# Kernel tuning notes

Measured on AMD Instinct MI355X. Metric: run time of the kernel, lower is better.

Reference implementation:

```python
import jax, jax.numpy as jnp
import numpy as np

N = 65536   # batch of (state, goal) pairs
S = 256     # s_dim
G = 128     # goal_dim
L = 128     # latent_dim (prior units[-1] == rvq dim)
A = 32      # action_dim
H = 512     # prior/posterior hidden
DH = 1024   # decoder hidden
Q = 8       # num residual quantizers
K = 1024    # codebook size


def setup_inputs() -> dict:
    key = jax.random.key(0)
    ks = jax.random.split(key, 16)

    def w(k, i, o):
        return jax.random.normal(k, (i, o), jnp.float32) * (1.0 / np.sqrt(i))

    return {
        "s": jax.random.normal(ks[0], (N, S), jnp.float32),
        "goal": jax.random.normal(ks[1], (N, G), jnp.float32),
        # PriorNet: S -> H -> H -> L (relu between, linear last)
        "pW0": w(ks[2], S, H), "pb0": jnp.zeros((H,), jnp.float32),
        "pW1": w(ks[3], H, H), "pb1": jnp.zeros((H,), jnp.float32),
        "pW2": w(ks[4], H, L), "pb2": jnp.zeros((L,), jnp.float32),
        # PosteriorNet: (S+G) -> H -> H -> L
        "qW0": w(ks[5], S + G, H), "qb0": jnp.zeros((H,), jnp.float32),
        "qW1": w(ks[6], H, H), "qb1": jnp.zeros((H,), jnp.float32),
        "qW2": w(ks[7], H, L), "qb2": jnp.zeros((L,), jnp.float32),
        # ActionDecoder: (S+L) -> DH -> DH (relu after each) -> mu_head A
        "dW0": w(ks[8], S + L, DH), "db0": jnp.zeros((DH,), jnp.float32),
        "dW1": w(ks[9], DH, DH), "db1": jnp.zeros((DH,), jnp.float32),
        "dW2": w(ks[10], DH, A), "db2": jnp.zeros((A,), jnp.float32),
        # per-quantizer codebooks [Q, K, L]
        "codebooks": jax.random.normal(ks[11], (Q, K, L), jnp.float32) * 0.02,
    }


def _rvq(y, codebooks):
    """Residual VQ with straight-through estimator.
    y: [N, L]; codebooks: [Q, K, L]. Returns (y_hat [N,L], loss_vq scalar)."""
    def step(carry, cb):
        residual, out = carry
        # argmin_k ||residual - cb[k]||^2 (drop the ||residual||^2 term)
        d = jnp.sum(cb * cb, axis=-1)[None, :] - 2.0 * (residual @ cb.T)  # [N, K]
        idx = jnp.argmin(d, axis=-1)                                       # [N]
        quant = cb[idx]                                                    # [N, L] gather
        quant_st = residual + jax.lax.stop_gradient(quant - residual)      # straight-through
        commit = jnp.mean((jax.lax.stop_gradient(quant) - residual) ** 2)  # commitment loss
        new_res = residual - jax.lax.stop_gradient(quant)
        return (new_res, out + quant_st), commit

    (_, y_hat), commits = jax.lax.scan(step, (y, jnp.zeros_like(y)), codebooks)
    return y_hat, jnp.sum(commits)


def reference(s, goal,
              pW0, pb0, pW1, pb1, pW2, pb2,
              qW0, qb0, qW1, qb1, qW2, qb2,
              dW0, db0, dW1, db1, dW2, db2,
              codebooks):
    relu = jax.nn.relu
    # prior: zp = f_theta(s)
    h = relu(s @ pW0 + pb0)
    h = relu(h @ pW1 + pb1)
    zp = h @ pW2 + pb2                                  # [N, L]
    # posterior: z = f_phi(s, goal)
    x = jnp.concatenate([s, goal], axis=-1)
    h = relu(x @ qW0 + qb0)
    h = relu(h @ qW1 + qb1)
    z = h @ qW2 + qb2                                   # [N, L]
    zp_sg = jax.lax.stop_gradient(zp)
    y = z - zp_sg
    y_hat, loss_vq = _rvq(y, codebooks)
    z_hat = y_hat + zp_sg
    # decoder: a_hat = pi_low(s, z_hat)
    xd = jnp.concatenate([s, z_hat], axis=-1)
    h = relu(xd @ dW0 + db0)
    h = relu(h @ dW1 + db1)
    a_hat = h @ dW2 + db2                               # [N, A]
    return a_hat
```

## Files before the change

kernel.cpp:

```cpp
#include <hip/hip_runtime.h>

#define NROWS 65536
typedef unsigned short u16;
typedef __attribute__((ext_vector_type(8))) short bf16x8;
typedef __attribute__((ext_vector_type(4))) float f32x4;

__device__ __forceinline__ u16 tobf(float v) {
    unsigned b = __float_as_uint(v);
    b += 0x7fffu + ((b >> 16) & 1u);
    return (u16)(b >> 16);
}
__device__ __forceinline__ float frombf(u16 h) {
    return __uint_as_float(((unsigned)h) << 16);
}
__device__ __forceinline__ void split2(float v, u16& h, u16& l) {
    h = tobf(v);
    l = tobf(v - frombf(h));
}

__global__ __launch_bounds__(256)
void wsplit(const float* __restrict__ W, u16* __restrict__ Th, u16* __restrict__ Tl,
            int K, int N)
{
    __shared__ float Tt[32][65];
    const int t = threadIdx.x;
    const int nb = blockIdx.x * 32, kb = blockIdx.y * 64;
    #pragma unroll
    for (int j = 0; j < 2; ++j) {
        int fi = j * 256 + t;
        int kk = fi >> 3;
        int n4 = (fi & 7) * 4;
        float4 v = *(const float4*)&W[(size_t)(kb + kk) * N + nb + n4];
        Tt[n4 + 0][kk] = v.x; Tt[n4 + 1][kk] = v.y;
        Tt[n4 + 2][kk] = v.z; Tt[n4 + 3][kk] = v.w;
    }
    __syncthreads();
    #pragma unroll
    for (int j = 0; j < 2; ++j) {
        int oi = j * 256 + t;
        int n  = oi >> 4;
        int k4 = (oi & 15) * 4;
        ushort4 h, l;
        split2(Tt[n][k4 + 0], h.x, l.x); split2(Tt[n][k4 + 1], h.y, l.y);
        split2(Tt[n][k4 + 2], h.z, l.z); split2(Tt[n][k4 + 3], h.w, l.w);
        size_t oa = (size_t)(nb + n) * K + kb + k4;
        *(ushort4*)(Th + oa) = h;
        *(ushort4*)(Tl + oa) = l;
    }
}

template<int FM, int FN, int NWX, int NWY, int RELU>
__global__ __launch_bounds__(256)
void gemm3(const float* __restrict__ A1, int w1,
           const float* __restrict__ A2, int w2,
           const u16* __restrict__ Wth, const u16* __restrict__ Wtl,
           const float* __restrict__ bias,
           float* __restrict__ C, int Kin, int Nout)
{
    constexpr int BM = NWY * FM * 16;
    constexpr int BN = NWX * FN * 16;
    constexpr int LDT = 40;
    static_assert(NWX * NWY == 4, "4 waves");
    __shared__ u16 Ah[BM * LDT], Al[BM * LDT], Bh[BN * LDT], Bl[BN * LDT];

    const int t = threadIdx.x, lane = t & 63, w = t >> 6;
    const int wx = w % NWX, wy = w / NWX;
    const int lg = lane >> 4, lm = lane & 15;
    const int rbase = blockIdx.y * BM, cbase = blockIdx.x * BN;

    f32x4 acc[FM][FN];
    #pragma unroll
    for (int i = 0; i < FM; ++i)
        #pragma unroll
        for (int j = 0; j < FN; ++j) acc[i][j] = (f32x4){0.f, 0.f, 0.f, 0.f};

    for (int kb = 0; kb < Kin; kb += 32) {
        #pragma unroll
        for (int j = 0; j < BM / 32; ++j) {
            int fi  = j * 256 + t;
            int row = fi >> 3;
            int k   = (fi & 7) * 4;
            int gc  = kb + k;
            const float* src = (gc < w1) ? (A1 + (size_t)(rbase + row) * w1 + gc)
                                         : (A2 + (size_t)(rbase + row) * w2 + (gc - w1));
            float4 v = *(const float4*)src;
            ushort4 h, l;
            split2(v.x, h.x, l.x); split2(v.y, h.y, l.y);
            split2(v.z, h.z, l.z); split2(v.w, h.w, l.w);
            *(ushort4*)&Ah[row * LDT + k] = h;
            *(ushort4*)&Al[row * LDT + k] = l;
        }
        #pragma unroll
        for (int j = 0; j < BN / 32; ++j) {
            int fi   = j * 256 + t;
            int nrow = fi >> 3;
            int k    = (fi & 7) * 4;
            size_t ga = (size_t)(cbase + nrow) * Kin + kb + k;
            *(ushort4*)&Bh[nrow * LDT + k] = *(const ushort4*)(Wth + ga);
            *(ushort4*)&Bl[nrow * LDT + k] = *(const ushort4*)(Wtl + ga);
        }
        __syncthreads();

        bf16x8 a_h[FM], a_l[FM], b_h[FN], b_l[FN];
        #pragma unroll
        for (int fm = 0; fm < FM; ++fm) {
            int off = (wy * FM * 16 + fm * 16 + lm) * LDT + lg * 8;
            a_h[fm] = *(const bf16x8*)&Ah[off];
            a_l[fm] = *(const bf16x8*)&Al[off];
        }
        #pragma unroll
        for (int fn = 0; fn < FN; ++fn) {
            int off = (wx * FN * 16 + fn * 16 + lm) * LDT + lg * 8;
            b_h[fn] = *(const bf16x8*)&Bh[off];
            b_l[fn] = *(const bf16x8*)&Bl[off];
        }
        #pragma unroll
        for (int fm = 0; fm < FM; ++fm)
            #pragma unroll
            for (int fn = 0; fn < FN; ++fn) {
                acc[fm][fn] = __builtin_amdgcn_mfma_f32_16x16x32_bf16(a_h[fm], b_h[fn], acc[fm][fn], 0, 0, 0);
                acc[fm][fn] = __builtin_amdgcn_mfma_f32_16x16x32_bf16(a_h[fm], b_l[fn], acc[fm][fn], 0, 0, 0);
                acc[fm][fn] = __builtin_amdgcn_mfma_f32_16x16x32_bf16(a_l[fm], b_h[fn], acc[fm][fn], 0, 0, 0);
            }
        __syncthreads();
    }

    float bn_[FN];
    #pragma unroll
    for (int fn = 0; fn < FN; ++fn)
        bn_[fn] = bias[cbase + wx * FN * 16 + fn * 16 + lm];
    #pragma unroll
    for (int fm = 0; fm < FM; ++fm)
        #pragma unroll
        for (int fn = 0; fn < FN; ++fn)
            #pragma unroll
            for (int r = 0; r < 4; ++r) {
                int m = rbase + wy * FM * 16 + fm * 16 + lg * 4 + r;
                int n = cbase + wx * FN * 16 + fn * 16 + lm;
                float v = acc[fm][fn][r] + bn_[fn];
                if (RELU) v = fmaxf(v, 0.f);
                C[(size_t)m * Nout + n] = v;
            }
}

__global__ __launch_bounds__(256)
void cbnorm_kernel(const float* __restrict__ cb, float* __restrict__ cbn)
{
    int code = blockIdx.x * 256 + threadIdx.x;
    const float* p = cb + (size_t)code * 128;
    float s = 0.f;
    #pragma unroll 8
    for (int d4 = 0; d4 < 32; ++d4) {
        float4 v = *(const float4*)(p + d4 * 4);
        s += v.x * v.x + v.y * v.y + v.z * v.z + v.w * v.w;
    }
    cbn[code] = s;
}

__global__ __launch_bounds__(256)
void cbsplit(const float* __restrict__ cb, u16* __restrict__ CBh, u16* __restrict__ CBl)
{
    int i = (blockIdx.x * 256 + threadIdx.x) * 4;
    float4 v = *(const float4*)(cb + i);
    ushort4 h, l;
    split2(v.x, h.x, l.x); split2(v.y, h.y, l.y);
    split2(v.z, h.z, l.z); split2(v.w, h.w, l.w);
    *(ushort4*)(CBh + i) = h;
    *(ushort4*)(CBl + i) = l;
}

#define RVQ_EPS 4e-3f

__device__ __forceinline__ float dot128(const float* __restrict__ r,
                                        const float* __restrict__ c)
{
    float s = 0.f;
    #pragma unroll 8
    for (int i = 0; i < 32; ++i) {
        float4 a = *(const float4*)(r + i * 4);
        float4 b = *(const float4*)(c + i * 4);
        s += a.x * b.x + a.y * b.y + a.z * b.z + a.w * b.w;
    }
    return s;
}

__global__ __launch_bounds__(256, 2)
void rvq_mfma(float* __restrict__ z, const float* __restrict__ zp,
              const float* __restrict__ cbf,
              const u16* __restrict__ CBh, const u16* __restrict__ CBl,
              const float* __restrict__ cbn,
              float* __restrict__ zhat )
{
    __shared__ float r_lds[64 * 132];
    __shared__ float cbn_lds[1024];
    __shared__ float red_m1[256];
    __shared__ int   red_k1[256];
    __shared__ float red_m2[256];
    __shared__ int   red_k2[256];
    __shared__ int   idx_sh[64];

    const int t = threadIdx.x, lane = t & 63, w = t >> 6;
    const int lm = lane & 15, lg = lane >> 4;
    const int rbase = blockIdx.x * 64;

    #pragma unroll
    for (int jj = 0; jj < 8; ++jj) {
        int f   = t + 256 * jj;
        int row = f >> 5;
        int c4  = (f & 31) << 2;
        float4 zv = *(const float4*)(z  + (size_t)(rbase + row) * 128 + c4);
        float4 pv = *(const float4*)(zp + (size_t)(rbase + row) * 128 + c4);
        float4 rv = make_float4(zv.x - pv.x, zv.y - pv.y, zv.z - pv.z, zv.w - pv.w);
        *(float4*)&r_lds[row * 132 + c4] = rv;
    }
    __syncthreads();

    for (int q = 0; q < 8; ++q) {
        {
            float4 v = *(const float4*)&cbn[q * 1024 + t * 4];
            *(float4*)&cbn_lds[t * 4] = v;
        }
        bf16x8 rh[4][4], rl[4][4];
        #pragma unroll
        for (int nt = 0; nt < 4; ++nt)
            #pragma unroll
            for (int ks = 0; ks < 4; ++ks) {
                const float* rp = &r_lds[(nt * 16 + lm) * 132 + ks * 32 + lg * 8];
                float4 v0 = *(const float4*)rp;
                float4 v1 = *(const float4*)(rp + 4);
                float fv[8] = { v0.x, v0.y, v0.z, v0.w, v1.x, v1.y, v1.z, v1.w };
                bf16x8 hh, ll;
                #pragma unroll
                for (int j = 0; j < 8; ++j) {
                    u16 h, l;
                    split2(fv[j], h, l);
                    hh[j] = (short)h; ll[j] = (short)l;
                }
                rh[nt][ks] = hh; rl[nt][ks] = ll;
            }
        __syncthreads();

        float m1[4], m2v[4];
        int   k1[4], k2[4];
        #pragma unroll
        for (int nt = 0; nt < 4; ++nt) { m1[nt] = 3.4e38f; m2v[nt] = 3.4e38f; k1[nt] = 0; k2[nt] = 0; }

        const int klo = w * 16 + lg * 4;
        for (int c = 0; c < 16; ++c) {
            int cbase = c * 64 + w * 16;
            bf16x8 ah[4], al[4];
            size_t gb = ((size_t)q * 1024 + cbase + lm) * 128 + lg * 8;
            #pragma unroll
            for (int ks = 0; ks < 4; ++ks) {
                ah[ks] = *(const bf16x8*)(CBh + gb + ks * 32);
                al[ks] = *(const bf16x8*)(CBl + gb + ks * 32);
            }
            float4 cbn4 = *(const float4*)&cbn_lds[cbase + lg * 4];

            #pragma unroll
            for (int nt = 0; nt < 4; ++nt) {
                f32x4 acc = (f32x4){0.f, 0.f, 0.f, 0.f};
                #pragma unroll
                for (int ks = 0; ks < 4; ++ks) {
                    acc = __builtin_amdgcn_mfma_f32_16x16x32_bf16(ah[ks], rh[nt][ks], acc, 0, 0, 0);
                    acc = __builtin_amdgcn_mfma_f32_16x16x32_bf16(ah[ks], rl[nt][ks], acc, 0, 0, 0);
                    acc = __builtin_amdgcn_mfma_f32_16x16x32_bf16(al[ks], rh[nt][ks], acc, 0, 0, 0);
                }
                float cbn_a[4] = { cbn4.x, cbn4.y, cbn4.z, cbn4.w };
                #pragma unroll
                for (int r = 0; r < 4; ++r) {
                    float d = fmaf(-2.f, acc[r], cbn_a[r]);
                    int  kk = c * 64 + klo + r;
                    bool lt1 = d < m1[nt];
                    bool lt2 = d < m2v[nt];
                    float nm2 = lt1 ? m1[nt] : (lt2 ? d : m2v[nt]);
                    int   nk2 = lt1 ? k1[nt] : (lt2 ? kk : k2[nt]);
                    if (lt1) { m1[nt] = d; k1[nt] = kk; }
                    m2v[nt] = nm2; k2[nt] = nk2;
                }
            }
        }

        #pragma unroll
        for (int nt = 0; nt < 4; ++nt) {
            #pragma unroll
            for (int st = 0; st < 2; ++st) {
                int msk = 16 << st;
                float om1 = __shfl_xor(m1[nt], msk);
                int   ok1 = __shfl_xor(k1[nt], msk);
                float om2 = __shfl_xor(m2v[nt], msk);
                int   ok2 = __shfl_xor(k2[nt], msk);
                bool aw = (m1[nt] < om1) || (m1[nt] == om1 && k1[nt] < ok1);
                float w1 = aw ? m1[nt] : om1;  int wk1 = aw ? k1[nt] : ok1;
                float l1 = aw ? om1 : m1[nt];  int lk1 = aw ? ok1 : k1[nt];
                float s2 = aw ? m2v[nt] : om2; int sk2 = aw ? k2[nt] : ok2;
                if (l1 < s2 || (l1 == s2 && lk1 < sk2)) { s2 = l1; sk2 = lk1; }
                m1[nt] = w1; k1[nt] = wk1; m2v[nt] = s2; k2[nt] = sk2;
            }
        }
        if (lane < 16) {
            #pragma unroll
            for (int nt = 0; nt < 4; ++nt) {
                int o = w * 64 + nt * 16 + lm;
                red_m1[o] = m1[nt]; red_k1[o] = k1[nt];
                red_m2[o] = m2v[nt]; red_k2[o] = k2[nt];
            }
        }
        __syncthreads();

        if (t < 64) {
            float M1 = 3.4e38f, M2 = 3.4e38f;
            int   K1 = 0x7fffffff, K2 = 0x7fffffff;
            #pragma unroll
            for (int ww = 0; ww < 4; ++ww) {
                int o = ww * 64 + t;
                float a1 = red_m1[o]; int b1 = red_k1[o];
                float a2 = red_m2[o]; int b2 = red_k2[o];
                if (a1 < M1 || (a1 == M1 && b1 < K1)) {
                    M2 = M1; K2 = K1; M1 = a1; K1 = b1;
                } else if (a1 < M2 || (a1 == M2 && b1 < K2)) { M2 = a1; K2 = b1; }
                if (a2 < M2 || (a2 == M2 && b2 < K2)) { M2 = a2; K2 = b2; }
            }
            int pick = K1;
            if (M2 - M1 <= RVQ_EPS) {
                const float* rrow = &r_lds[t * 132];
                float d1 = cbn_lds[K1] - 2.f * dot128(rrow, cbf + ((size_t)q * 1024 + K1) * 128);
                float d2 = cbn_lds[K2] - 2.f * dot128(rrow, cbf + ((size_t)q * 1024 + K2) * 128);
                if (d2 < d1 || (d2 == d1 && K2 < K1)) pick = K2;
            }
            idx_sh[t] = pick;
        }
        __syncthreads();

        #pragma unroll
        for (int jj = 0; jj < 8; ++jj) {
            int f   = t + 256 * jj;
            int row = f >> 5;
            int c4  = (f & 31) << 2;
            int k   = idx_sh[row];
            float4 v = *(const float4*)(cbf + ((size_t)q * 1024 + k) * 128 + c4);
            float4* rp = (float4*)&r_lds[row * 132 + c4];
            float4 rv = *rp;
            rv.x -= v.x; rv.y -= v.y; rv.z -= v.z; rv.w -= v.w;
            *rp = rv;
        }
        __syncthreads();
    }

    #pragma unroll
    for (int jj = 0; jj < 8; ++jj) {
        int f   = t + 256 * jj;
        int row = f >> 5;
        int c4  = (f & 31) << 2;
        float4 zv = *(const float4*)(z + (size_t)(rbase + row) * 128 + c4);
        float4 rv = *(float4*)&r_lds[row * 132 + c4];
        float4 o = make_float4(zv.x - rv.x, zv.y - rv.y, zv.z - rv.z, zv.w - rv.w);
        *(float4*)(zhat + (size_t)(rbase + row) * 128 + c4) = o;
    }
}

extern "C" void kernel_launch(void* const* d_in, const int* in_sizes, int n_in,
                              void* d_out, int out_size, void* d_ws, size_t ws_size,
                              hipStream_t stream)
{
    const float* s    = (const float*)d_in[0];
    const float* goal = (const float*)d_in[1];
    const float* Wp[9]  = { (const float*)d_in[2],  (const float*)d_in[4],  (const float*)d_in[6],
                            (const float*)d_in[8],  (const float*)d_in[10], (const float*)d_in[12],
                            (const float*)d_in[14], (const float*)d_in[16], (const float*)d_in[18] };
    const float* Bp[9]  = { (const float*)d_in[3],  (const float*)d_in[5],  (const float*)d_in[7],
                            (const float*)d_in[9],  (const float*)d_in[11], (const float*)d_in[13],
                            (const float*)d_in[15], (const float*)d_in[17], (const float*)d_in[19] };
    const float* cb   = (const float*)d_in[20];
    float* out = (float*)d_out;

    static const int WK[9] = { 256, 512, 512, 384, 512, 512, 384, 1024, 1024 };
    static const int WN[9] = { 512, 512, 128, 512, 512, 128, 1024, 1024, 32 };
    size_t woff[10]; woff[0] = 0;
    for (int i = 0; i < 9; ++i) woff[i + 1] = woff[i] + (size_t)WK[i] * WN[i];

    float* zp  = (float*)d_ws;
    float* zz  = zp + (size_t)NROWS * 128;
    float* cbn = zz + (size_t)NROWS * 128;
    u16*  Wth  = (u16*)(cbn + 8192);
    u16*  Wtl  = Wth + woff[9];
    u16*  CBh  = Wtl + woff[9];
    u16*  CBl  = CBh + 1048576;
    uintptr_t bA = ((uintptr_t)(CBl + 1048576) + 255) & ~(uintptr_t)255;
    float* bufA = (float*)bA;

    size_t used = (size_t)(bA - (uintptr_t)d_ws);
    size_t avail = (ws_size > used) ? (ws_size - used) : 0;
    size_t ch = avail / (2 * 1024 * sizeof(float));
    if (ch > NROWS) ch = NROWS;
    ch &= ~(size_t)127;
    if (ch < 128) ch = 128;
    const int CH = (int)ch;
    float* bufB = bufA + (size_t)CH * 1024;

    dim3 blk(256);

    cbnorm_kernel<<<32, blk, 0, stream>>>(cb, cbn);
    cbsplit<<<1024, blk, 0, stream>>>(cb, CBh, CBl);
    for (int i = 0; i < 9; ++i)
        wsplit<<<dim3(WN[i] / 32, WK[i] / 64), blk, 0, stream>>>(Wp[i], Wth + woff[i], Wtl + woff[i], WK[i], WN[i]);

    for (int off = 0; off < NROWS; off += CH) {
        int rows = (NROWS - off) < CH ? (NROWS - off) : CH;
        int gy = rows / 128;
        const float* sC = s + (size_t)off * 256;
        const float* gC = goal + (size_t)off * 128;
        gemm3<4,4,2,2,1><<<dim3(4, gy), blk, 0, stream>>>(sC, 256, nullptr, 0, Wth + woff[0], Wtl + woff[0], Bp[0], bufA, 256, 512);
        gemm3<4,4,2,2,1><<<dim3(4, gy), blk, 0, stream>>>(bufA, 512, nullptr, 0, Wth + woff[1], Wtl + woff[1], Bp[1], bufB, 512, 512);
        gemm3<4,4,2,2,0><<<dim3(1, gy), blk, 0, stream>>>(bufB, 512, nullptr, 0, Wth + woff[2], Wtl + woff[2], Bp[2], zp + (size_t)off * 128, 512, 128);
        gemm3<4,4,2,2,1><<<dim3(4, gy), blk, 0, stream>>>(sC, 256, gC, 128, Wth + woff[3], Wtl + woff[3], Bp[3], bufA, 384, 512);
        gemm3<4,4,2,2,1><<<dim3(4, gy), blk, 0, stream>>>(bufA, 512, nullptr, 0, Wth + woff[4], Wtl + woff[4], Bp[4], bufB, 512, 512);
        gemm3<4,4,2,2,0><<<dim3(1, gy), blk, 0, stream>>>(bufB, 512, nullptr, 0, Wth + woff[5], Wtl + woff[5], Bp[5], zz + (size_t)off * 128, 512, 128);
    }

    rvq_mfma<<<NROWS / 64, blk, 0, stream>>>(zz, zp, cb, CBh, CBl, cbn, zz);

    for (int off = 0; off < NROWS; off += CH) {
        int rows = (NROWS - off) < CH ? (NROWS - off) : CH;
        int gy = rows / 128;
        const float* sC = s + (size_t)off * 256;
        const float* zC = zz + (size_t)off * 128;
        gemm3<4,4,2,2,1><<<dim3(8, gy), blk, 0, stream>>>(sC, 256, zC, 128, Wth + woff[6], Wtl + woff[6], Bp[6], bufA, 384, 1024);
        gemm3<4,4,2,2,1><<<dim3(8, gy), blk, 0, stream>>>(bufA, 1024, nullptr, 0, Wth + woff[7], Wtl + woff[7], Bp[7], bufB, 1024, 1024);
        gemm3<2,2,1,4,0><<<dim3(1, gy), blk, 0, stream>>>(bufB, 1024, nullptr, 0, Wth + woff[8], Wtl + woff[8], Bp[8], out + (size_t)off * 32, 1024, 32);
    }
}
```

Baseline: 2.792 ms.

## Double-buffer GEMM A tiles, load weights straight to registers, drop RVQ LDS staging

The GEMM kernel now double-buffers the activation tile in LDS and prefetches the next K-slice into registers while MFMAs run. Weight fragments are read directly from global memory into registers rather than staged through LDS, which leaves one barrier per step instead of two. In the RVQ kernel the codebook-norm LDS copy and a barrier are removed in favour of direct global reads, the occupancy hint is dropped, and s_setprio is raised around the MFMA chain. The direct global weight loads may be less coalesced, and without the occupancy hint the compiler may use more registers.

```diff
diff --git a/kernel.cpp b/kernel.cpp
--- a/kernel.cpp
+++ b/kernel.cpp
@@ -16,6 +16,12 @@
 __device__ __forceinline__ void split2(float v, u16& h, u16& l) {
     h = tobf(v);
     l = tobf(v - frombf(h));
+}
+
+__device__ __forceinline__ void bar_lgkm() {
+    asm volatile("s_waitcnt lgkmcnt(0)" ::: "memory");
+    __builtin_amdgcn_s_barrier();
+    __builtin_amdgcn_sched_barrier(0);
 }
 
 __global__ __launch_bounds__(256)
@@ -60,8 +66,9 @@
     constexpr int BM = NWY * FM * 16;
     constexpr int BN = NWX * FN * 16;
     constexpr int LDT = 40;
+    constexpr int AIT = BM / 32;
     static_assert(NWX * NWY == 4, "4 waves");
-    __shared__ u16 Ah[BM * LDT], Al[BM * LDT], Bh[BN * LDT], Bl[BN * LDT];
+    __shared__ u16 Ah[2][BM * LDT], Al[2][BM * LDT];
 
     const int t = threadIdx.x, lane = t & 63, w = t >> 6;
     const int wx = w % NWX, wy = w / NWX;
@@ -74,45 +81,56 @@
         #pragma unroll
         for (int j = 0; j < FN; ++j) acc[i][j] = (f32x4){0.f, 0.f, 0.f, 0.f};
 
-    for (int kb = 0; kb < Kin; kb += 32) {
-        #pragma unroll
-        for (int j = 0; j < BM / 32; ++j) {
+    float4 av[AIT];
+
+    auto loadA = [&](int kb) {
+        #pragma unroll
+        for (int j = 0; j < AIT; ++j) {
             int fi  = j * 256 + t;
             int row = fi >> 3;
             int k   = (fi & 7) * 4;
             int gc  = kb + k;
             const float* src = (gc < w1) ? (A1 + (size_t)(rbase + row) * w1 + gc)
                                          : (A2 + (size_t)(rbase + row) * w2 + (gc - w1));
-            float4 v = *(const float4*)src;
+            av[j] = *(const float4*)src;
+        }
+    };
+    auto writeA = [&](int b) {
+        #pragma unroll
+        for (int j = 0; j < AIT; ++j) {
+            int fi  = j * 256 + t;
+            int row = fi >> 3;
+            int k   = (fi & 7) * 4;
             ushort4 h, l;
-            split2(v.x, h.x, l.x); split2(v.y, h.y, l.y);
-            split2(v.z, h.z, l.z); split2(v.w, h.w, l.w);
-            *(ushort4*)&Ah[row * LDT + k] = h;
-            *(ushort4*)&Al[row * LDT + k] = l;
-        }
-        #pragma unroll
-        for (int j = 0; j < BN / 32; ++j) {
-            int fi   = j * 256 + t;
-            int nrow = fi >> 3;
-            int k    = (fi & 7) * 4;
-            size_t ga = (size_t)(cbase + nrow) * Kin + kb + k;
-            *(ushort4*)&Bh[nrow * LDT + k] = *(const ushort4*)(Wth + ga);
-            *(ushort4*)&Bl[nrow * LDT + k] = *(const ushort4*)(Wtl + ga);
-        }
-        __syncthreads();
-
-        bf16x8 a_h[FM], a_l[FM], b_h[FN], b_l[FN];
+            split2(av[j].x, h.x, l.x); split2(av[j].y, h.y, l.y);
+            split2(av[j].z, h.z, l.z); split2(av[j].w, h.w, l.w);
+            *(ushort4*)&Ah[b][row * LDT + k] = h;
+            *(ushort4*)&Al[b][row * LDT + k] = l;
+        }
+    };
+
+    loadA(0);
+    writeA(0);
+    bar_lgkm();
+
+    const int NSTEP = Kin / 32;
+    for (int ti = 0; ti < NSTEP; ++ti) {
+        bf16x8 b_h[FN], b_l[FN];
+        #pragma unroll
+        for (int fn = 0; fn < FN; ++fn) {
+            size_t ga = (size_t)(cbase + wx * FN * 16 + fn * 16 + lm) * Kin + ti * 32 + lg * 8;
+            b_h[fn] = *(const bf16x8*)(Wth + ga);
+            b_l[fn] = *(const bf16x8*)(Wtl + ga);
+        }
+        if (ti + 1 < NSTEP) loadA((ti + 1) * 32);
+
+        const int b = ti & 1;
+        bf16x8 a_h[FM], a_l[FM];
         #pragma unroll
         for (int fm = 0; fm < FM; ++fm) {
             int off = (wy * FM * 16 + fm * 16 + lm) * LDT + lg * 8;
-            a_h[fm] = *(const bf16x8*)&Ah[off];
-            a_l[fm] = *(const bf16x8*)&Al[off];
-        }
-        #pragma unroll
-        for (int fn = 0; fn < FN; ++fn) {
-            int off = (wx * FN * 16 + fn * 16 + lm) * LDT + lg * 8;
-            b_h[fn] = *(const bf16x8*)&Bh[off];
-            b_l[fn] = *(const bf16x8*)&Bl[off];
+            a_h[fm] = *(const bf16x8*)&Ah[b][off];
+            a_l[fm] = *(const bf16x8*)&Al[b][off];
         }
         #pragma unroll
         for (int fm = 0; fm < FM; ++fm)
@@ -122,7 +140,9 @@
                 acc[fm][fn] = __builtin_amdgcn_mfma_f32_16x16x32_bf16(a_h[fm], b_l[fn], acc[fm][fn], 0, 0, 0);
                 acc[fm][fn] = __builtin_amdgcn_mfma_f32_16x16x32_bf16(a_l[fm], b_h[fn], acc[fm][fn], 0, 0, 0);
             }
-        __syncthreads();
+
+        if (ti + 1 < NSTEP) writeA((ti + 1) & 1);
+        bar_lgkm();
     }
 
     float bn_[FN];
@@ -184,7 +204,7 @@
     return s;
 }
 
-__global__ __launch_bounds__(256, 2)
+__global__ __launch_bounds__(256)
 void rvq_mfma(float* __restrict__ z, const float* __restrict__ zp,
               const float* __restrict__ cbf,
               const u16* __restrict__ CBh, const u16* __restrict__ CBl,
@@ -192,7 +212,6 @@
               float* __restrict__ zhat )
 {
     __shared__ float r_lds[64 * 132];
-    __shared__ float cbn_lds[1024];
     __shared__ float red_m1[256];
     __shared__ int   red_k1[256];
     __shared__ float red_m2[256];
@@ -216,10 +235,6 @@
     __syncthreads();
 
     for (int q = 0; q < 8; ++q) {
-        {
-            float4 v = *(const float4*)&cbn[q * 1024 + t * 4];
-            *(float4*)&cbn_lds[t * 4] = v;
-        }
         bf16x8 rh[4][4], rl[4][4];
         #pragma unroll
         for (int nt = 0; nt < 4; ++nt)
@@ -238,7 +253,6 @@
                 }
                 rh[nt][ks] = hh; rl[nt][ks] = ll;
             }
-        __syncthreads();
 
         float m1[4], m2v[4];
         int   k1[4], k2[4];
@@ -247,25 +261,27 @@
 
         const int klo = w * 16 + lg * 4;
         for (int c = 0; c < 16; ++c) {
-            int cbase = c * 64 + w * 16;
+            int cb0 = c * 64 + w * 16;
             bf16x8 ah[4], al[4];
-            size_t gb = ((size_t)q * 1024 + cbase + lm) * 128 + lg * 8;
+            size_t gb = ((size_t)q * 1024 + cb0 + lm) * 128 + lg * 8;
             #pragma unroll
             for (int ks = 0; ks < 4; ++ks) {
                 ah[ks] = *(const bf16x8*)(CBh + gb + ks * 32);
                 al[ks] = *(const bf16x8*)(CBl + gb + ks * 32);
             }
-            float4 cbn4 = *(const float4*)&cbn_lds[cbase + lg * 4];
+            float4 cbn4 = *(const float4*)(cbn + q * 1024 + cb0 + lg * 4);
 
             #pragma unroll
             for (int nt = 0; nt < 4; ++nt) {
                 f32x4 acc = (f32x4){0.f, 0.f, 0.f, 0.f};
+                __builtin_amdgcn_s_setprio(1);
                 #pragma unroll
                 for (int ks = 0; ks < 4; ++ks) {
                     acc = __builtin_amdgcn_mfma_f32_16x16x32_bf16(ah[ks], rh[nt][ks], acc, 0, 0, 0);
                     acc = __builtin_amdgcn_mfma_f32_16x16x32_bf16(ah[ks], rl[nt][ks], acc, 0, 0, 0);
                     acc = __builtin_amdgcn_mfma_f32_16x16x32_bf16(al[ks], rh[nt][ks], acc, 0, 0, 0);
                 }
+                __builtin_amdgcn_s_setprio(0);
                 float cbn_a[4] = { cbn4.x, cbn4.y, cbn4.z, cbn4.w };
                 #pragma unroll
                 for (int r = 0; r < 4; ++r) {
@@ -324,8 +340,8 @@
             int pick = K1;
             if (M2 - M1 <= RVQ_EPS) {
                 const float* rrow = &r_lds[t * 132];
-                float d1 = cbn_lds[K1] - 2.f * dot128(rrow, cbf + ((size_t)q * 1024 + K1) * 128);
-                float d2 = cbn_lds[K2] - 2.f * dot128(rrow, cbf + ((size_t)q * 1024 + K2) * 128);
+                float d1 = cbn[q * 1024 + K1] - 2.f * dot128(rrow, cbf + ((size_t)q * 1024 + K1) * 128);
+                float d2 = cbn[q * 1024 + K2] - 2.f * dot128(rrow, cbf + ((size_t)q * 1024 + K2) * 128);
                 if (d2 < d1 || (d2 == d1 && K2 < K1)) pick = K2;
             }
             idx_sh[t] = pick;
```

Result: slower. 3.086 ms (+10.5%).

## Shrink RVQ block to 32 rows with pre-split bf16 fragments in LDS

Applied to the files above, without the earlier changes.

The RVQ kernel now handles 32 rows per block instead of 64, doubling the grid and raising the launch-bounds occupancy hint to 4 blocks per CU. The hi/lo bf16 split of the residual is written once into LDS in MFMA fragment order, refreshed during the residual update, rather than recomputed from fp32 at the top of every quantizer step. Codebook norms are read straight from global memory instead of staged in LDS. This cuts register pressure and per-step conversion work, but each block now reloads the whole codebook for half as many rows, doubling codebook traffic.

```diff
diff --git a/kernel.cpp b/kernel.cpp
--- a/kernel.cpp
+++ b/kernel.cpp
@@ -184,27 +184,26 @@
     return s;
 }
 
-__global__ __launch_bounds__(256, 2)
+__global__ __launch_bounds__(256, 4)
 void rvq_mfma(float* __restrict__ z, const float* __restrict__ zp,
               const float* __restrict__ cbf,
               const u16* __restrict__ CBh, const u16* __restrict__ CBl,
               const float* __restrict__ cbn,
               float* __restrict__ zhat )
 {
-    __shared__ float r_lds[64 * 132];
-    __shared__ float cbn_lds[1024];
-    __shared__ float red_m1[256];
-    __shared__ int   red_k1[256];
-    __shared__ float red_m2[256];
-    __shared__ int   red_k2[256];
-    __shared__ int   idx_sh[64];
+    __shared__ float r_lds[32 * 132];
+    __shared__ u16   fh[512 * 8];
+    __shared__ u16   fl[512 * 8];
+    __shared__ float red_m1[128], red_m2[128];
+    __shared__ int   red_k1[128], red_k2[128];
+    __shared__ int   idx_sh[32];
 
     const int t = threadIdx.x, lane = t & 63, w = t >> 6;
     const int lm = lane & 15, lg = lane >> 4;
-    const int rbase = blockIdx.x * 64;
-
-    #pragma unroll
-    for (int jj = 0; jj < 8; ++jj) {
+    const int rbase = blockIdx.x * 32;
+
+    #pragma unroll
+    for (int jj = 0; jj < 4; ++jj) {
         int f   = t + 256 * jj;
         int row = f >> 5;
         int c4  = (f & 31) << 2;
@@ -214,75 +213,85 @@
         *(float4*)&r_lds[row * 132 + c4] = rv;
     }
     __syncthreads();
+    #pragma unroll
+    for (int jj = 0; jj < 4; ++jj) {
+        int f   = t + 256 * jj;
+        int row = f & 31;
+        int c4  = (f >> 5) << 2;
+        float4 rv = *(float4*)&r_lds[row * 132 + c4];
+        int nt = row >> 4, lmr = row & 15;
+        int ks = c4 >> 5, lgr = (c4 >> 3) & 3, off = c4 & 7;
+        int chunk = ((nt * 4 + ks) * 4 + lgr) * 16 + lmr;
+        ushort4 h, l;
+        split2(rv.x, h.x, l.x); split2(rv.y, h.y, l.y);
+        split2(rv.z, h.z, l.z); split2(rv.w, h.w, l.w);
+        *(ushort4*)&fh[chunk * 8 + off] = h;
+        *(ushort4*)&fl[chunk * 8 + off] = l;
+    }
+    __syncthreads();
 
     for (int q = 0; q < 8; ++q) {
-        {
-            float4 v = *(const float4*)&cbn[q * 1024 + t * 4];
-            *(float4*)&cbn_lds[t * 4] = v;
-        }
-        bf16x8 rh[4][4], rl[4][4];
-        #pragma unroll
-        for (int nt = 0; nt < 4; ++nt)
+        bf16x8 rhf[2][4], rlf[2][4];
+        #pragma unroll
+        for (int nt = 0; nt < 2; ++nt)
             #pragma unroll
             for (int ks = 0; ks < 4; ++ks) {
-                const float* rp = &r_lds[(nt * 16 + lm) * 132 + ks * 32 + lg * 8];
-                float4 v0 = *(const float4*)rp;
-                float4 v1 = *(const float4*)(rp + 4);
-                float fv[8] = { v0.x, v0.y, v0.z, v0.w, v1.x, v1.y, v1.z, v1.w };
-                bf16x8 hh, ll;
-                #pragma unroll
-                for (int j = 0; j < 8; ++j) {
-                    u16 h, l;
-                    split2(fv[j], h, l);
-                    hh[j] = (short)h; ll[j] = (short)l;
-                }
-                rh[nt][ks] = hh; rl[nt][ks] = ll;
-            }
-        __syncthreads();
-
-        float m1[4], m2v[4];
-        int   k1[4], k2[4];
-        #pragma unroll
-        for (int nt = 0; nt < 4; ++nt) { m1[nt] = 3.4e38f; m2v[nt] = 3.4e38f; k1[nt] = 0; k2[nt] = 0; }
+                int chunk = (nt * 4 + ks) * 64 + lane;
+                rhf[nt][ks] = *(const bf16x8*)&fh[chunk * 8];
+                rlf[nt][ks] = *(const bf16x8*)&fl[chunk * 8];
+            }
+
+        float m1[2], m2v[2];
+        int   k1[2], k2[2];
+        #pragma unroll
+        for (int nt = 0; nt < 2; ++nt) { m1[nt] = 3.4e38f; m2v[nt] = 3.4e38f; k1[nt] = 0; k2[nt] = 0; }
 
         const int klo = w * 16 + lg * 4;
         for (int c = 0; c < 16; ++c) {
-            int cbase = c * 64 + w * 16;
-            bf16x8 ah[4], al[4];
-            size_t gb = ((size_t)q * 1024 + cbase + lm) * 128 + lg * 8;
+            int cb0 = c * 64 + w * 16;
+            size_t gb = ((size_t)q * 1024 + cb0 + lm) * 128;
+            float4 cbn4 = *(const float4*)(cbn + q * 1024 + cb0 + lg * 4);
+
+            f32x4 acc0 = (f32x4){0.f, 0.f, 0.f, 0.f};
+            f32x4 acc1 = (f32x4){0.f, 0.f, 0.f, 0.f};
             #pragma unroll
             for (int ks = 0; ks < 4; ++ks) {
-                ah[ks] = *(const bf16x8*)(CBh + gb + ks * 32);
-                al[ks] = *(const bf16x8*)(CBl + gb + ks * 32);
-            }
-            float4 cbn4 = *(const float4*)&cbn_lds[cbase + lg * 4];
-
-            #pragma unroll
-            for (int nt = 0; nt < 4; ++nt) {
-                f32x4 acc = (f32x4){0.f, 0.f, 0.f, 0.f};
-                #pragma unroll
-                for (int ks = 0; ks < 4; ++ks) {
-                    acc = __builtin_amdgcn_mfma_f32_16x16x32_bf16(ah[ks], rh[nt][ks], acc, 0, 0, 0);
-                    acc = __builtin_amdgcn_mfma_f32_16x16x32_bf16(ah[ks], rl[nt][ks], acc, 0, 0, 0);
-                    acc = __builtin_amdgcn_mfma_f32_16x16x32_bf16(al[ks], rh[nt][ks], acc, 0, 0, 0);
+                bf16x8 ah = *(const bf16x8*)(CBh + gb + ks * 32 + lg * 8);
+                bf16x8 al = *(const bf16x8*)(CBl + gb + ks * 32 + lg * 8);
+                acc0 = __builtin_amdgcn_mfma_f32_16x16x32_bf16(ah, rhf[0][ks], acc0, 0, 0, 0);
+                acc0 = __builtin_amdgcn_mfma_f32_16x16x32_bf16(ah, rlf[0][ks], acc0, 0, 0, 0);
+                acc0 = __builtin_amdgcn_mfma_f32_16x16x32_bf16(al, rhf[0][ks], acc0, 0, 0, 0);
+                acc1 = __builtin_amdgcn_mfma_f32_16x16x32_bf16(ah, rhf[1][ks], acc1, 0, 0, 0);
+                acc1 = __builtin_amdgcn_mfma_f32_16x16x32_bf16(ah, rlf[1][ks], acc1, 0, 0, 0);
+                acc1 = __builtin_amdgcn_mfma_f32_16x16x32_bf16(al, rhf[1][ks], acc1, 0, 0, 0);
+            }
+            float cbn_a[4] = { cbn4.x, cbn4.y, cbn4.z, cbn4.w };
+            #pragma unroll
+            for (int r = 0; r < 4; ++r) {
+                int kk = c * 64 + klo + r;
+                {
+                    float d = fmaf(-2.f, acc0[r], cbn_a[r]);
+                    bool lt1 = d < m1[0];
+                    bool lt2 = d < m2v[0];
+                    float nm2 = lt1 ? m1[0] : (lt2 ? d : m2v[0]);
+                    int   nk2 = lt1 ? k1[0] : (lt2 ? kk : k2[0]);
+                    if (lt1) { m1[0] = d; k1[0] = kk; }
+                    m2v[0] = nm2; k2[0] = nk2;
                 }
-                float cbn_a[4] = { cbn4.x, cbn4.y, cbn4.z, cbn4.w };
-                #pragma unroll
-                for (int r = 0; r < 4; ++r) {
-                    float d = fmaf(-2.f, acc[r], cbn_a[r]);
-                    int  kk = c * 64 + klo + r;
-                    bool lt1 = d < m1[nt];
-                    bool lt2 = d < m2v[nt];
-                    float nm2 = lt1 ? m1[nt] : (lt2 ? d : m2v[nt]);
-                    int   nk2 = lt1 ? k1[nt] : (lt2 ? kk : k2[nt]);
-                    if (lt1) { m1[nt] = d; k1[nt] = kk; }
-                    m2v[nt] = nm2; k2[nt] = nk2;
+                {
+                    float d = fmaf(-2.f, acc1[r], cbn_a[r]);
+                    bool lt1 = d < m1[1];
+                    bool lt2 = d < m2v[1];
+                    float nm2 = lt1 ? m1[1] : (lt2 ? d : m2v[1]);
+                    int   nk2 = lt1 ? k1[1] : (lt2 ? kk : k2[1]);
+                    if (lt1) { m1[1] = d; k1[1] = kk; }
+                    m2v[1] = nm2; k2[1] = nk2;
                 }
             }
         }
 
         #pragma unroll
-        for (int nt = 0; nt < 4; ++nt) {
+        for (int nt = 0; nt < 2; ++nt) {
             #pragma unroll
             for (int st = 0; st < 2; ++st) {
                 int msk = 16 << st;
@@ -300,20 +309,20 @@
         }
         if (lane < 16) {
             #pragma unroll
-            for (int nt = 0; nt < 4; ++nt) {
-                int o = w * 64 + nt * 16 + lm;
+            for (int nt = 0; nt < 2; ++nt) {
+                int o = w * 32 + nt * 16 + lm;
                 red_m1[o] = m1[nt]; red_k1[o] = k1[nt];
                 red_m2[o] = m2v[nt]; red_k2[o] = k2[nt];
             }
         }
         __syncthreads();
 
-        if (t < 64) {
+        if (t < 32) {
             float M1 = 3.4e38f, M2 = 3.4e38f;
             int   K1 = 0x7fffffff, K2 = 0x7fffffff;
             #pragma unroll
             for (int ww = 0; ww < 4; ++ww) {
-                int o = ww * 64 + t;
+                int o = ww * 32 + t;
                 float a1 = red_m1[o]; int b1 = red_k1[o];
                 float a2 = red_m2[o]; int b2 = red_k2[o];
                 if (a1 < M1 || (a1 == M1 && b1 < K1)) {
@@ -324,8 +333,8 @@
             int pick = K1;
             if (M2 - M1 <= RVQ_EPS) {
                 const float* rrow = &r_lds[t * 132];
-                float d1 = cbn_lds[K1] - 2.f * dot128(rrow, cbf + ((size_t)q * 1024 + K1) * 128);
-                float d2 = cbn_lds[K2] - 2.f * dot128(rrow, cbf + ((size_t)q * 1024 + K2) * 128);
+                float d1 = cbn[q * 1024 + K1] - 2.f * dot128(rrow, cbf + ((size_t)q * 1024 + K1) * 128);
+                float d2 = cbn[q * 1024 + K2] - 2.f * dot128(rrow, cbf + ((size_t)q * 1024 + K2) * 128);
                 if (d2 < d1 || (d2 == d1 && K2 < K1)) pick = K2;
             }
             idx_sh[t] = pick;
@@ -333,22 +342,32 @@
         __syncthreads();
 
         #pragma unroll
-        for (int jj = 0; jj < 8; ++jj) {
+        for (int jj = 0; jj < 4; ++jj) {
             int f   = t + 256 * jj;
-            int row = f >> 5;
-            int c4  = (f & 31) << 2;
+            int row = f & 31;
+            int c4  = (f >> 5) << 2;
             int k   = idx_sh[row];
             float4 v = *(const float4*)(cbf + ((size_t)q * 1024 + k) * 128 + c4);
             float4* rp = (float4*)&r_lds[row * 132 + c4];
             float4 rv = *rp;
             rv.x -= v.x; rv.y -= v.y; rv.z -= v.z; rv.w -= v.w;
             *rp = rv;
+            if (q < 7) {
+                int nt = row >> 4, lmr = row & 15;
+                int ks = c4 >> 5, lgr = (c4 >> 3) & 3, off = c4 & 7;
+                int chunk = ((nt * 4 + ks) * 4 + lgr) * 16 + lmr;
+                ushort4 h, l;
+                split2(rv.x, h.x, l.x); split2(rv.y, h.y, l.y);
+                split2(rv.z, h.z, l.z); split2(rv.w, h.w, l.w);
+                *(ushort4*)&fh[chunk * 8 + off] = h;
+                *(ushort4*)&fl[chunk * 8 + off] = l;
+            }
         }
         __syncthreads();
     }
 
     #pragma unroll
-    for (int jj = 0; jj < 8; ++jj) {
+    for (int jj = 0; jj < 4; ++jj) {
         int f   = t + 256 * jj;
         int row = f >> 5;
         int c4  = (f & 31) << 2;
@@ -418,7 +437,7 @@
         gemm3<4,4,2,2,0><<<dim3(1, gy), blk, 0, stream>>>(bufB, 512, nullptr, 0, Wth + woff[5], Wtl + woff[5], Bp[5], zz + (size_t)off * 128, 512, 128);
     }
 
-    rvq_mfma<<<NROWS / 64, blk, 0, stream>>>(zz, zp, cb, CBh, CBl, cbn, zz);
+    rvq_mfma<<<NROWS / 32, blk, 0, stream>>>(zz, zp, cb, CBh, CBl, cbn, zz);
 
     for (int off = 0; off < NROWS; off += CH) {
         int rows = (NROWS - off) < CH ? (NROWS - off) : CH;
```

Result: slower. 2.954 ms (+5.8%).
